# Optimization experiments

Hardware: AMD Instinct MI355X
Metric: run time of the kernel (lower is better)

The kernel has to match this reference:

```python
import jax, jax.numpy as jnp
import numpy as np

L, D, F, V = 24, 1024, 4096, 50277  # n_layer, n_embd, ffn hidden (4*D), vocab
RESCALE = 6


def _ln(x, w, b, eps=1e-5):
    m = jnp.mean(x, axis=-1, keepdims=True)
    v = jnp.mean(jnp.square(x - m), axis=-1, keepdims=True)
    return (x - m) * jax.lax.rsqrt(v + eps) * w + b


def setup_inputs() -> dict:
    key = jax.random.key(0)
    ks = iter(jax.random.split(key, 64))

    def nrm(shape, s=0.02):
        return jax.random.normal(next(ks), shape, jnp.float32) * s

    def uni(shape):
        return jax.random.uniform(next(ks), shape, jnp.float32)

    state = jnp.zeros((L, 5, D), jnp.float32).at[:, 4, :].set(-1e30)  # pp init
    return {
        "token_embd": jax.random.normal(next(ks), (D,), jnp.float32),
        "state": state,
        "emb_ln_w": jnp.ones((D,), jnp.float32),
        "emb_ln_b": jnp.zeros((D,), jnp.float32),
        "ln1_w": jnp.ones((L, D), jnp.float32),
        "ln1_b": jnp.zeros((L, D), jnp.float32),
        "ln2_w": jnp.ones((L, D), jnp.float32),
        "ln2_b": jnp.zeros((L, D), jnp.float32),
        "att_tmk": uni((L, D)),
        "att_tmv": uni((L, D)),
        "att_tmr": uni((L, D)),
        "att_tf": nrm((L, D), 0.5),
        "att_td": -jnp.exp(nrm((L, D), 0.5)),  # time_decay = -exp(w) at load
        "att_kw": nrm((L, D, D)),
        "att_vw": nrm((L, D, D)),
        "att_rw": nrm((L, D, D)),
        "att_ow": nrm((L, D, D)),
        "ffn_tmk": uni((L, D)),
        "ffn_tmr": uni((L, D)),
        "ffn_kw": nrm((L, F, D)),
        "ffn_vw": nrm((L, D, F)),
        "ffn_rw": nrm((L, D, D)),
        "out_ln_w": jnp.ones((D,), jnp.float32),
        "out_ln_b": jnp.zeros((D,), jnp.float32),
        "head_w": nrm((V, D)),
    }


def reference(token_embd, state, emb_ln_w, emb_ln_b, ln1_w, ln1_b, ln2_w, ln2_b,
              att_tmk, att_tmv, att_tmr, att_tf, att_td, att_kw, att_vw, att_rw,
              att_ow, ffn_tmk, ffn_tmr, ffn_kw, ffn_vw, ffn_rw,
              out_ln_w, out_ln_b, head_w):
    x0 = _ln(token_embd, emb_ln_w, emb_ln_b)  # encoder

    def layer(x, inputs):
        (i, st, l1w, l1b, l2w, l2b, tmk, tmv, tmr, tf, td,
         kw, vw, rw, ow, ftmk, ftmr, fkw, fvw, frw) = inputs
        # ---- time mixing ----
        xn = _ln(x, l1w, l1b)
        s_att, aa, bb, pp = st[1], st[2], st[3], st[4]
        xk = xn * tmk + s_att * (1 - tmk)
        xv = xn * tmv + s_att * (1 - tmv)
        xr = xn * tmr + s_att * (1 - tmr)
        r = jax.nn.sigmoid(rw @ xr)
        kk = kw @ xk
        vv = vw @ xv
        ww = tf + kk
        p = jnp.maximum(pp, ww)
        e1 = jnp.exp(pp - p)
        e2 = jnp.exp(ww - p)
        a = e1 * aa + e2 * vv
        b = e1 * bb + e2
        ww2 = pp + td
        p2 = jnp.maximum(ww2, kk)
        f1 = jnp.exp(ww2 - p2)
        f2 = jnp.exp(kk - p2)
        new_aa = f1 * aa + f2 * vv
        new_bb = f1 * bb + f2
        x = x + ow @ (r * (a / b))
        # ---- channel mixing ----
        xn2 = _ln(x, l2w, l2b)
        s_ffn = st[0]
        xk2 = xn2 * ftmk + s_ffn * (1 - ftmk)
        xr2 = xn2 * ftmr + s_ffn * (1 - ftmr)
        r2 = jax.nn.sigmoid(frw @ xr2)
        k2 = jnp.square(jax.nn.relu(fkw @ xk2))
        x = x + r2 * (fvw @ k2)
        # rescale every RESCALE layers
        x = jnp.where((i + 1) % RESCALE == 0, x * 0.5, x)
        new_st = jnp.stack([xn2, xn, new_aa, new_bb, p2])
        return x, new_st

    idx = jnp.arange(L)
    x, new_state = jax.lax.scan(
        layer, x0,
        (idx, state, ln1_w, ln1_b, ln2_w, ln2_b, att_tmk, att_tmv, att_tmr,
         att_tf, att_td, att_kw, att_vw, att_rw, att_ow, ffn_tmk, ffn_tmr,
         ffn_kw, ffn_vw, ffn_rw))
    logits = head_w @ _ln(x, out_ln_w, out_ln_b)  # decoder
    return logits, new_state
```

## Files before the change

kernel.cpp:

```cpp
#include <hip/hip_runtime.h>

#define DD 1024
#define FF 4096
#define LL 24
#define VV 50277
#define PFB 256

typedef float v4f __attribute__((ext_vector_type(4)));


__device__ __forceinline__ float wave_sum(float v) {
#pragma unroll
    for (int o = 32; o > 0; o >>= 1) v += __shfl_xor(v, o, 64);
    return v;
}

__device__ __forceinline__ float block_sum(float v, float* scr) {
    v = wave_sum(v);
    int w = threadIdx.x >> 6;
    __syncthreads();
    if ((threadIdx.x & 63) == 0) scr[w] = v;
    __syncthreads();
    return scr[0] + scr[1] + scr[2] + scr[3];
}

__device__ __forceinline__ v4f ln_vec(v4f xv, const float* __restrict__ w,
                                      const float* __restrict__ b, float* scr, int t) {
    float m = block_sum(xv[0] + xv[1] + xv[2] + xv[3], scr) * (1.0f / 1024.0f);
    v4f d = xv - m;
    float var = block_sum(d[0]*d[0] + d[1]*d[1] + d[2]*d[2] + d[3]*d[3], scr) * (1.0f / 1024.0f);
    float rs = rsqrtf(var + 1e-5f);
    v4f w4 = ((const v4f*)w)[t], b4 = ((const v4f*)b)[t];
    return d * rs * w4 + b4;
}

__device__ __forceinline__ v4f mixv(v4f n, v4f s, v4f m) { return n * m + s * (1.0f - m); }

__device__ __forceinline__ float dotv(v4f a, v4f x) {
    return fmaf(a[0], x[0], fmaf(a[1], x[1], fmaf(a[2], x[2], a[3] * x[3])));
}

struct Row { v4f a, b, c, d; };

__device__ __forceinline__ void row_load(Row& r, const float* p, int lane) {
    const v4f* q = (const v4f*)p;
    r.a = q[lane]; r.b = q[lane + 64]; r.c = q[lane + 128]; r.d = q[lane + 192];
}
__device__ __forceinline__ float row_dot(const Row& r, const v4f* v, int lane) {
    return dotv(r.a, v[lane]) + dotv(r.b, v[lane + 64]) +
           dotv(r.c, v[lane + 128]) + dotv(r.d, v[lane + 192]);
}


__device__ __forceinline__ void pf_region(const float* p, int nvec, int pb, int t) {
    if (p == nullptr || nvec <= 0) return;
    const v4f* q = (const v4f*)p;
    int chunk = (nvec + PFB - 1) / PFB;
    int lo = pb * chunk;
    int end = lo + chunk; if (end > nvec) end = nvec;
    int i = lo + t;
    v4f a0 = {0,0,0,0}, a1 = a0, a2 = a0, a3 = a0, a4 = a0, a5 = a0, a6 = a0, a7 = a0;
    for (; i + 1792 < end; i += 2048) {
        v4f t0 = q[i],        t1 = q[i + 256],  t2 = q[i + 512],  t3 = q[i + 768];
        v4f t4 = q[i + 1024], t5 = q[i + 1280], t6 = q[i + 1536], t7 = q[i + 1792];
        a0 += t0; a1 += t1; a2 += t2; a3 += t3;
        a4 += t4; a5 += t5; a6 += t6; a7 += t7;
    }
    for (; i < end; i += 256) a0 += q[i];
    a0 = (a0 + a1) + (a2 + a3) + ((a4 + a5) + (a6 + a7));
    asm volatile("" :: "v"(a0));
}


__global__ __launch_bounds__(256) void k1_timemix(
    const float* __restrict__ xin, const float* __restrict__ st,
    const float* __restrict__ enc_w, const float* __restrict__ enc_b,
    const float* __restrict__ l1w, const float* __restrict__ l1b,
    const float* __restrict__ tmk, const float* __restrict__ tmv,
    const float* __restrict__ tmr,
    const float* __restrict__ kw, const float* __restrict__ vw,
    const float* __restrict__ rw,
    float* __restrict__ kk, float* __restrict__ vv, float* __restrict__ rr,
    float* __restrict__ x0out, float* __restrict__ st_out,
    const float* pfa, int na, const float* pfb, int nb) {
    const int t = threadIdx.x;
    int b = blockIdx.x;
    if (b < PFB) { pf_region(pfa, na, b, t); pf_region(pfb, nb, b, t); return; }
    b -= PFB;
    __shared__ __align__(16) float s_k[DD], s_v[DD], s_r[DD];
    __shared__ float scr[4];
    const int lane = t & 63, w = t >> 6;

    v4f xv = ((const v4f*)xin)[t];
    if (enc_w) xv = ln_vec(xv, enc_w, enc_b, scr, t);
    if (x0out && b == 0) ((v4f*)x0out)[t] = xv;
    v4f n = ln_vec(xv, l1w, l1b, scr, t);
    if (b == 0) ((v4f*)(st_out + DD))[t] = n;
    {
        v4f sa = ((const v4f*)(st + DD))[t];
        ((v4f*)s_k)[t] = mixv(n, sa, ((const v4f*)tmk)[t]);
        ((v4f*)s_v)[t] = mixv(n, sa, ((const v4f*)tmv)[t]);
        ((v4f*)s_r)[t] = mixv(n, sa, ((const v4f*)tmr)[t]);
    }
    __syncthreads();

    const int ridx = b * 4 + w, m = ridx >> 10, row = ridx & 1023;
    Row W;
    row_load(W, (m == 0 ? kw : m == 1 ? vw : rw) + (size_t)row * DD, lane);
    const v4f* vec = (const v4f*)(m == 0 ? s_k : m == 1 ? s_v : s_r);
    float acc = wave_sum(row_dot(W, vec, lane));
    if (lane == 0) {
        if (m == 0)      kk[row] = acc;
        else if (m == 1) vv[row] = acc;
        else             rr[row] = 1.0f / (1.0f + expf(-acc));
    }
}


__global__ __launch_bounds__(256) void k2_wkv_out(
    const float* __restrict__ st, const float* __restrict__ tf,
    const float* __restrict__ td,
    const float* __restrict__ kk, const float* __restrict__ vv,
    const float* __restrict__ rr, const float* __restrict__ ow,
    float* __restrict__ x, float* __restrict__ st_out,
    const float* pfa, int na, const float* pfb, int nb) {
    const int t = threadIdx.x;
    int b = blockIdx.x;
    if (b < PFB) { pf_region(pfa, na, b, t); pf_region(pfb, nb, b, t); return; }
    b -= PFB;
    __shared__ __align__(16) float rab[DD];
    const int lane = t & 63, w = t >> 6;

    {
        v4f kx = ((const v4f*)kk)[t];
        v4f vx = ((const v4f*)vv)[t];
        v4f rx = ((const v4f*)rr)[t];
        v4f aa = ((const v4f*)(st + 2 * DD))[t];
        v4f bb = ((const v4f*)(st + 3 * DD))[t];
        v4f pp = ((const v4f*)(st + 4 * DD))[t];
        v4f tf4 = ((const v4f*)tf)[t];
        v4f td4 = ((const v4f*)td)[t];
        v4f rb, naa, nbb, np2;
#pragma unroll
        for (int c = 0; c < 4; ++c) {
            float kc = kx[c], vc = vx[c];
            float wwc = tf4[c] + kc;
            float p = fmaxf(pp[c], wwc);
            float e1 = expf(pp[c] - p), e2 = expf(wwc - p);
            rb[c] = rx[c] * ((e1 * aa[c] + e2 * vc) / (e1 * bb[c] + e2));
            float ww2 = pp[c] + td4[c];
            float p2 = fmaxf(ww2, kc);
            float f1 = expf(ww2 - p2), f2 = expf(kc - p2);
            naa[c] = f1 * aa[c] + f2 * vc;
            nbb[c] = f1 * bb[c] + f2;
            np2[c] = p2;
        }
        ((v4f*)rab)[t] = rb;
        if (b == 0) {
            ((v4f*)(st_out + 2 * DD))[t] = naa;
            ((v4f*)(st_out + 3 * DD))[t] = nbb;
            ((v4f*)(st_out + 4 * DD))[t] = np2;
        }
    }
    __syncthreads();

    const int row = b * 4 + w;
    Row W;
    row_load(W, ow + (size_t)row * DD, lane);
    float acc = wave_sum(row_dot(W, (const v4f*)rab, lane));
    if (lane == 0) x[row] += acc;
}


__global__ __launch_bounds__(256) void k3_ffn_kr(
    const float* __restrict__ x, const float* __restrict__ st,
    const float* __restrict__ l2w, const float* __restrict__ l2b,
    const float* __restrict__ ftmk, const float* __restrict__ ftmr,
    const float* __restrict__ fkw, const float* __restrict__ frw,
    float* __restrict__ k2, float* __restrict__ r2, float* __restrict__ st_out,
    const float* pfa, int na, const float* pfb, int nb) {
    const int t = threadIdx.x;
    int b = blockIdx.x;
    if (b < PFB) { pf_region(pfa, na, b, t); pf_region(pfb, nb, b, t); return; }
    b -= PFB;
    __shared__ __align__(16) float s_k[DD], s_r[DD];
    __shared__ float scr[4];
    const int lane = t & 63, w = t >> 6;

    v4f xv = ((const v4f*)x)[t];
    v4f n = ln_vec(xv, l2w, l2b, scr, t);
    if (b == 0) ((v4f*)st_out)[t] = n;
    {
        v4f sf = ((const v4f*)st)[t];
        ((v4f*)s_k)[t] = mixv(n, sf, ((const v4f*)ftmk)[t]);
        ((v4f*)s_r)[t] = mixv(n, sf, ((const v4f*)ftmr)[t]);
    }
    __syncthreads();

    const int ridx = b * 4 + w;
    const float* Wp;
    const v4f* vec;
    if (ridx < FF) { Wp = fkw + (size_t)ridx * DD; vec = (const v4f*)s_k; }
    else           { Wp = frw + (size_t)(ridx - FF) * DD; vec = (const v4f*)s_r; }
    Row W;
    row_load(W, Wp, lane);
    float acc = wave_sum(row_dot(W, vec, lane));
    if (lane == 0) {
        if (ridx < FF) { float rl = fmaxf(acc, 0.f); k2[ridx] = rl * rl; }
        else           r2[ridx - FF] = 1.0f / (1.0f + expf(-acc));
    }
}


__global__ __launch_bounds__(256) void k4_ffn_v(
    const float* __restrict__ fvw, const float* __restrict__ k2,
    const float* __restrict__ r2, float* __restrict__ x, float scale,
    const float* pfa, int na, const float* pfb, int nb) {
    const int t = threadIdx.x;
    int b = blockIdx.x;
    if (b < PFB) { pf_region(pfa, na, b, t); pf_region(pfb, nb, b, t); return; }
    b -= PFB;
    __shared__ __align__(16) float k2s[FF];
    const int lane = t & 63, w = t >> 6;
#pragma unroll
    for (int j = 0; j < 4; ++j)
        ((v4f*)k2s)[t + 256 * j] = ((const v4f*)k2)[t + 256 * j];
    __syncthreads();

    const int row = b * 4 + w;
    const v4f* W4 = (const v4f*)(fvw + (size_t)row * FF);
    const v4f* v4 = (const v4f*)k2s;
    float acc = 0.f;
#pragma unroll
    for (int j = 0; j < 16; ++j) {
        v4f a = W4[lane + 64 * j];
        v4f bx = v4[lane + 64 * j];
        acc = fmaf(a[0], bx[0], fmaf(a[1], bx[1], fmaf(a[2], bx[2], fmaf(a[3], bx[3], acc))));
    }
    acc = wave_sum(acc);
    if (lane == 0) x[row] = (x[row] + r2[row] * acc) * scale;
}


__global__ __launch_bounds__(256) void k_head(const float* __restrict__ head_w,
                                              const float* __restrict__ x,
                                              const float* __restrict__ olw,
                                              const float* __restrict__ olb,
                                              float* __restrict__ logits) {
    __shared__ __align__(16) float xs[DD];
    __shared__ float scr[4];
    const int t = threadIdx.x, lane = t & 63, w = t >> 6;
    const int row = blockIdx.x * 4 + w;
    Row W;
    if (row < VV) row_load(W, head_w + (size_t)row * DD, lane);
    v4f xv = ((const v4f*)x)[t];
    v4f nx = ln_vec(xv, olw, olb, scr, t);
    ((v4f*)xs)[t] = nx;
    __syncthreads();
    if (row < VV) {
        float acc = wave_sum(row_dot(W, (const v4f*)xs, lane));
        if (lane == 0) logits[row] = acc;
    }
}


extern "C" void kernel_launch(void* const* d_in, const int* in_sizes, int n_in,
                              void* d_out, int out_size, void* d_ws, size_t ws_size,
                              hipStream_t stream) {
    const float* token_embd = (const float*)d_in[0];
    const float* state      = (const float*)d_in[1];
    const float* emb_ln_w   = (const float*)d_in[2];
    const float* emb_ln_b   = (const float*)d_in[3];
    const float* ln1_w      = (const float*)d_in[4];
    const float* ln1_b      = (const float*)d_in[5];
    const float* ln2_w      = (const float*)d_in[6];
    const float* ln2_b      = (const float*)d_in[7];
    const float* att_tmk    = (const float*)d_in[8];
    const float* att_tmv    = (const float*)d_in[9];
    const float* att_tmr    = (const float*)d_in[10];
    const float* att_tf     = (const float*)d_in[11];
    const float* att_td     = (const float*)d_in[12];
    const float* att_kw     = (const float*)d_in[13];
    const float* att_vw     = (const float*)d_in[14];
    const float* att_rw     = (const float*)d_in[15];
    const float* att_ow     = (const float*)d_in[16];
    const float* ffn_tmk    = (const float*)d_in[17];
    const float* ffn_tmr    = (const float*)d_in[18];
    const float* ffn_kw     = (const float*)d_in[19];
    const float* ffn_vw     = (const float*)d_in[20];
    const float* ffn_rw     = (const float*)d_in[21];
    const float* out_ln_w   = (const float*)d_in[22];
    const float* out_ln_b   = (const float*)d_in[23];
    const float* head_w     = (const float*)d_in[24];

    float* logits = (float*)d_out;
    float* st_out_base = (float*)d_out + VV;

    float* ws  = (float*)d_ws;
    float* x   = ws;
    float* kk  = ws + 1024;
    float* vv  = ws + 2048;
    float* rr  = ws + 3072;
    float* k2b = ws + 4096;
    float* r2b = ws + 8192;

    const int V_D   = DD * DD / 4;
    const int V_FKH = FF * DD / 8;

    for (int i = 0; i < LL; ++i) {
        const float* st = state + (size_t)i * 5 * DD;
        float* sto = st_out_base + (size_t)i * 5 * DD;
        const float* kw_i  = att_kw + (size_t)i * DD * DD;
        const float* vw_i  = att_vw + (size_t)i * DD * DD;
        const float* rw_i  = att_rw + (size_t)i * DD * DD;
        const float* ow_i  = att_ow + (size_t)i * DD * DD;
        const float* fkw_i = ffn_kw + (size_t)i * FF * DD;
        const float* fvw_i = ffn_vw + (size_t)i * DD * FF;
        const float* frw_i = ffn_rw + (size_t)i * DD * DD;
        const bool last = (i == LL - 1);

        k1_timemix<<<PFB + 768, 256, 0, stream>>>(
            (i == 0) ? token_embd : x, st,
            (i == 0) ? emb_ln_w : nullptr, (i == 0) ? emb_ln_b : nullptr,
            ln1_w + i * DD, ln1_b + i * DD,
            att_tmk + i * DD, att_tmv + i * DD, att_tmr + i * DD,
            kw_i, vw_i, rw_i, kk, vv, rr,
            (i == 0) ? x : nullptr, sto,
            ow_i, V_D, fkw_i, V_FKH);

        k2_wkv_out<<<PFB + 256, 256, 0, stream>>>(
            st, att_tf + i * DD, att_td + i * DD, kk, vv, rr, ow_i, x, sto,
            fkw_i + (size_t)FF * DD / 2, V_FKH, frw_i, V_D);

        k3_ffn_kr<<<PFB + 1280, 256, 0, stream>>>(
            x, st, ln2_w + i * DD, ln2_b + i * DD,
            ffn_tmk + i * DD, ffn_tmr + i * DD, fkw_i, frw_i,
            k2b, r2b, sto,
            fvw_i, 2 * V_FKH,
            last ? nullptr : rw_i + DD * DD, last ? 0 : V_D);

        float scale = ((i + 1) % 6 == 0) ? 0.5f : 1.0f;
        k4_ffn_v<<<PFB + 256, 256, 0, stream>>>(
            fvw_i, k2b, r2b, x, scale,
            last ? nullptr : kw_i + DD * DD, last ? 0 : V_D,
            last ? nullptr : vw_i + DD * DD, last ? 0 : V_D);
    }

    k_head<<<(VV + 3) / 4, 256, 0, stream>>>(head_w, x, out_ln_w, out_ln_b, logits);
}
```

Baseline: 722.5 us.

## Fuse RWKV layer into two kernels with split-K atomics, drop prefetch blocks

Each layer's four kernels become two. kA computes the k/v/r projections, the WKV update and the output projection for a column slice, accumulating into per-layer buffers with atomics. kB fuses the FFN key/receptance matvecs with a column-sliced value matvec, also accumulated with atomics. The residual update is deferred into the next kernel's prologue, and the L2 prefetch blocks are removed. LayerNorm moves to a one-pass sum and sum-of-squares reduction. This cuts launches and intermediate round trips, at the cost of float atomics and a less numerically stable variance.

```diff
diff --git a/kernel.cpp b/kernel.cpp
--- a/kernel.cpp
+++ b/kernel.cpp
@@ -4,7 +4,6 @@
 #define FF 4096
 #define LL 24
 #define VV 50277
-#define PFB 256
 
 typedef float v4f __attribute__((ext_vector_type(4)));
 
@@ -15,23 +14,26 @@
     return v;
 }
 
-__device__ __forceinline__ float block_sum(float v, float* scr) {
-    v = wave_sum(v);
-    int w = threadIdx.x >> 6;
-    __syncthreads();
-    if ((threadIdx.x & 63) == 0) scr[w] = v;
-    __syncthreads();
-    return scr[0] + scr[1] + scr[2] + scr[3];
-}
-
-__device__ __forceinline__ v4f ln_vec(v4f xv, const float* __restrict__ w,
-                                      const float* __restrict__ b, float* scr, int t) {
-    float m = block_sum(xv[0] + xv[1] + xv[2] + xv[3], scr) * (1.0f / 1024.0f);
-    v4f d = xv - m;
-    float var = block_sum(d[0]*d[0] + d[1]*d[1] + d[2]*d[2] + d[3]*d[3], scr) * (1.0f / 1024.0f);
+template <int NW>
+__device__ __forceinline__ v4f ln_fast(v4f x, const float* __restrict__ w,
+                                       const float* __restrict__ b,
+                                       float* scr, int t, bool act) {
+    float s1 = act ? (x[0] + x[1] + x[2] + x[3]) : 0.f;
+    float s2 = act ? (x[0]*x[0] + x[1]*x[1] + x[2]*x[2] + x[3]*x[3]) : 0.f;
+    s1 = wave_sum(s1); s2 = wave_sum(s2);
+    int wv = t >> 6;
+    __syncthreads();
+    if ((t & 63) == 0) { scr[wv] = s1; scr[NW + wv] = s2; }
+    __syncthreads();
+    float S1 = 0.f, S2 = 0.f;
+#pragma unroll
+    for (int i = 0; i < NW; ++i) { S1 += scr[i]; S2 += scr[NW + i]; }
+    float m = S1 * (1.0f / 1024.0f);
+    float var = S2 * (1.0f / 1024.0f) - m * m;
     float rs = rsqrtf(var + 1e-5f);
-    v4f w4 = ((const v4f*)w)[t], b4 = ((const v4f*)b)[t];
-    return d * rs * w4 + b4;
+    v4f w4 = act ? ((const v4f*)w)[t] : (v4f){0.f, 0.f, 0.f, 0.f};
+    v4f b4 = act ? ((const v4f*)b)[t] : (v4f){0.f, 0.f, 0.f, 0.f};
+    return (x - m) * rs * w4 + b4;
 }
 
 __device__ __forceinline__ v4f mixv(v4f n, v4f s, v4f m) { return n * m + s * (1.0f - m); }
@@ -52,213 +54,167 @@
 }
 
 
-__device__ __forceinline__ void pf_region(const float* p, int nvec, int pb, int t) {
-    if (p == nullptr || nvec <= 0) return;
-    const v4f* q = (const v4f*)p;
-    int chunk = (nvec + PFB - 1) / PFB;
-    int lo = pb * chunk;
-    int end = lo + chunk; if (end > nvec) end = nvec;
-    int i = lo + t;
-    v4f a0 = {0,0,0,0}, a1 = a0, a2 = a0, a3 = a0, a4 = a0, a5 = a0, a6 = a0, a7 = a0;
-    for (; i + 1792 < end; i += 2048) {
-        v4f t0 = q[i],        t1 = q[i + 256],  t2 = q[i + 512],  t3 = q[i + 768];
-        v4f t4 = q[i + 1024], t5 = q[i + 1280], t6 = q[i + 1536], t7 = q[i + 1792];
-        a0 += t0; a1 += t1; a2 += t2; a3 += t3;
-        a4 += t4; a5 += t5; a6 += t6; a7 += t7;
-    }
-    for (; i < end; i += 256) a0 += q[i];
-    a0 = (a0 + a1) + (a2 + a3) + ((a4 + a5) + (a6 + a7));
-    asm volatile("" :: "v"(a0));
-}
-
-
-__global__ __launch_bounds__(256) void k1_timemix(
-    const float* __restrict__ xin, const float* __restrict__ st,
+__global__ __launch_bounds__(768, 3) void kA(
+    const float* __restrict__ xprev, const float* __restrict__ a1p,
+    const float* __restrict__ r2p, const float* __restrict__ sp, float scale_prev,
     const float* __restrict__ enc_w, const float* __restrict__ enc_b,
+    const float* __restrict__ st,
     const float* __restrict__ l1w, const float* __restrict__ l1b,
     const float* __restrict__ tmk, const float* __restrict__ tmv,
-    const float* __restrict__ tmr,
+    const float* __restrict__ tmr, const float* __restrict__ tf,
+    const float* __restrict__ td,
     const float* __restrict__ kw, const float* __restrict__ vw,
-    const float* __restrict__ rw,
-    float* __restrict__ kk, float* __restrict__ vv, float* __restrict__ rr,
-    float* __restrict__ x0out, float* __restrict__ st_out,
-    const float* pfa, int na, const float* pfb, int nb) {
-    const int t = threadIdx.x;
-    int b = blockIdx.x;
-    if (b < PFB) { pf_region(pfa, na, b, t); pf_region(pfb, nb, b, t); return; }
-    b -= PFB;
-    __shared__ __align__(16) float s_k[DD], s_v[DD], s_r[DD];
-    __shared__ float scr[4];
-    const int lane = t & 63, w = t >> 6;
-
-    v4f xv = ((const v4f*)xin)[t];
-    if (enc_w) xv = ln_vec(xv, enc_w, enc_b, scr, t);
-    if (x0out && b == 0) ((v4f*)x0out)[t] = xv;
-    v4f n = ln_vec(xv, l1w, l1b, scr, t);
-    if (b == 0) ((v4f*)(st_out + DD))[t] = n;
-    {
+    const float* __restrict__ rw, const float* __restrict__ ow,
+    float* __restrict__ A1i, float* __restrict__ xbuf_i, float* __restrict__ sto) {
+    __shared__ __align__(16) v4f s_mix[3][256];
+    __shared__ float kvrL[3][4];
+    __shared__ __align__(16) float rabL[4];
+    __shared__ float scr[24];
+    const int t = threadIdx.x, lane = t & 63, w = t >> 6, b = blockIdx.x;
+
+    const int m = w >> 2, ch4 = w & 3;
+    Row R;
+    row_load(R, (m == 0 ? kw : m == 1 ? vw : rw) + (size_t)(4 * b + ch4) * DD, lane);
+    v4f ow0 = *(const v4f*)(ow + (size_t)t * DD + 4 * b);
+    v4f ow1;
+    if (t < 256) ow1 = *(const v4f*)(ow + (size_t)(768 + t) * DD + 4 * b);
+
+    v4f xin = {0.f, 0.f, 0.f, 0.f};
+    if (t < 256) {
+        v4f xp = ((const v4f*)xprev)[t];
+        if (enc_w == nullptr) {
+            v4f a1 = ((const v4f*)a1p)[t];
+            v4f r2 = ((const v4f*)r2p)[t];
+            v4f s  = ((const v4f*)sp)[t];
+            xin = (xp + a1 + r2 * s) * scale_prev;
+        } else xin = xp;
+    }
+    if (enc_w) xin = ln_fast<12>(xin, enc_w, enc_b, scr, t, t < 256);
+
+    v4f xn = ln_fast<12>(xin, l1w, l1b, scr, t, t < 256);
+    if (t < 256) {
+        if (b == 0) {
+            ((v4f*)(sto + DD))[t] = xn;
+            ((v4f*)xbuf_i)[t] = xin;
+        }
         v4f sa = ((const v4f*)(st + DD))[t];
-        ((v4f*)s_k)[t] = mixv(n, sa, ((const v4f*)tmk)[t]);
-        ((v4f*)s_v)[t] = mixv(n, sa, ((const v4f*)tmv)[t]);
-        ((v4f*)s_r)[t] = mixv(n, sa, ((const v4f*)tmr)[t]);
-    }
-    __syncthreads();
-
-    const int ridx = b * 4 + w, m = ridx >> 10, row = ridx & 1023;
-    Row W;
-    row_load(W, (m == 0 ? kw : m == 1 ? vw : rw) + (size_t)row * DD, lane);
-    const v4f* vec = (const v4f*)(m == 0 ? s_k : m == 1 ? s_v : s_r);
-    float acc = wave_sum(row_dot(W, vec, lane));
-    if (lane == 0) {
-        if (m == 0)      kk[row] = acc;
-        else if (m == 1) vv[row] = acc;
-        else             rr[row] = 1.0f / (1.0f + expf(-acc));
-    }
-}
-
-
-__global__ __launch_bounds__(256) void k2_wkv_out(
-    const float* __restrict__ st, const float* __restrict__ tf,
-    const float* __restrict__ td,
-    const float* __restrict__ kk, const float* __restrict__ vv,
-    const float* __restrict__ rr, const float* __restrict__ ow,
-    float* __restrict__ x, float* __restrict__ st_out,
-    const float* pfa, int na, const float* pfb, int nb) {
-    const int t = threadIdx.x;
-    int b = blockIdx.x;
-    if (b < PFB) { pf_region(pfa, na, b, t); pf_region(pfb, nb, b, t); return; }
-    b -= PFB;
-    __shared__ __align__(16) float rab[DD];
-    const int lane = t & 63, w = t >> 6;
-
-    {
-        v4f kx = ((const v4f*)kk)[t];
-        v4f vx = ((const v4f*)vv)[t];
-        v4f rx = ((const v4f*)rr)[t];
-        v4f aa = ((const v4f*)(st + 2 * DD))[t];
-        v4f bb = ((const v4f*)(st + 3 * DD))[t];
-        v4f pp = ((const v4f*)(st + 4 * DD))[t];
-        v4f tf4 = ((const v4f*)tf)[t];
-        v4f td4 = ((const v4f*)td)[t];
-        v4f rb, naa, nbb, np2;
-#pragma unroll
-        for (int c = 0; c < 4; ++c) {
-            float kc = kx[c], vc = vx[c];
-            float wwc = tf4[c] + kc;
-            float p = fmaxf(pp[c], wwc);
-            float e1 = expf(pp[c] - p), e2 = expf(wwc - p);
-            rb[c] = rx[c] * ((e1 * aa[c] + e2 * vc) / (e1 * bb[c] + e2));
-            float ww2 = pp[c] + td4[c];
-            float p2 = fmaxf(ww2, kc);
-            float f1 = expf(ww2 - p2), f2 = expf(kc - p2);
-            naa[c] = f1 * aa[c] + f2 * vc;
-            nbb[c] = f1 * bb[c] + f2;
-            np2[c] = p2;
-        }
-        ((v4f*)rab)[t] = rb;
-        if (b == 0) {
-            ((v4f*)(st_out + 2 * DD))[t] = naa;
-            ((v4f*)(st_out + 3 * DD))[t] = nbb;
-            ((v4f*)(st_out + 4 * DD))[t] = np2;
-        }
-    }
-    __syncthreads();
-
-    const int row = b * 4 + w;
-    Row W;
-    row_load(W, ow + (size_t)row * DD, lane);
-    float acc = wave_sum(row_dot(W, (const v4f*)rab, lane));
-    if (lane == 0) x[row] += acc;
-}
-
-
-__global__ __launch_bounds__(256) void k3_ffn_kr(
-    const float* __restrict__ x, const float* __restrict__ st,
+        s_mix[0][t] = mixv(xn, sa, ((const v4f*)tmk)[t]);
+        s_mix[1][t] = mixv(xn, sa, ((const v4f*)tmv)[t]);
+        s_mix[2][t] = mixv(xn, sa, ((const v4f*)tmr)[t]);
+    }
+    __syncthreads();
+
+    {
+        float acc = wave_sum(row_dot(R, &s_mix[m][0], lane));
+        if (lane == 0) kvrL[m][ch4] = acc;
+    }
+    __syncthreads();
+
+    if (t < 4) {
+        const int c = 4 * b + t;
+        float kk = kvrL[0][t], vv = kvrL[1][t];
+        float rr = 1.0f / (1.0f + expf(-kvrL[2][t]));
+        float aa = st[2 * DD + c], bb = st[3 * DD + c], pp = st[4 * DD + c];
+        float tfv = tf[c], tdv = td[c];
+        float ww = tfv + kk;
+        float p = fmaxf(pp, ww);
+        float e1 = expf(pp - p), e2 = expf(ww - p);
+        rabL[t] = rr * ((e1 * aa + e2 * vv) / (e1 * bb + e2));
+        float ww2 = pp + tdv;
+        float p2 = fmaxf(ww2, kk);
+        float f1 = expf(ww2 - p2), f2 = expf(kk - p2);
+        sto[2 * DD + c] = f1 * aa + f2 * vv;
+        sto[3 * DD + c] = f1 * bb + f2;
+        sto[4 * DD + c] = p2;
+    }
+    __syncthreads();
+
+    {
+        v4f rab4 = *(const v4f*)rabL;
+        atomicAdd(&A1i[t], dotv(ow0, rab4));
+        if (t < 256) atomicAdd(&A1i[768 + t], dotv(ow1, rab4));
+    }
+}
+
+
+__global__ __launch_bounds__(256, 2) void kB(
+    const float* __restrict__ xbuf_i, const float* __restrict__ A1i,
+    const float* __restrict__ st,
     const float* __restrict__ l2w, const float* __restrict__ l2b,
     const float* __restrict__ ftmk, const float* __restrict__ ftmr,
-    const float* __restrict__ fkw, const float* __restrict__ frw,
-    float* __restrict__ k2, float* __restrict__ r2, float* __restrict__ st_out,
-    const float* pfa, int na, const float* pfb, int nb) {
-    const int t = threadIdx.x;
-    int b = blockIdx.x;
-    if (b < PFB) { pf_region(pfa, na, b, t); pf_region(pfb, nb, b, t); return; }
-    b -= PFB;
-    __shared__ __align__(16) float s_k[DD], s_r[DD];
-    __shared__ float scr[4];
-    const int lane = t & 63, w = t >> 6;
-
-    v4f xv = ((const v4f*)x)[t];
-    v4f n = ln_vec(xv, l2w, l2b, scr, t);
-    if (b == 0) ((v4f*)st_out)[t] = n;
+    const float* __restrict__ fkw, const float* __restrict__ fvw,
+    const float* __restrict__ frw,
+    float* __restrict__ Si, float* __restrict__ r2o, float* __restrict__ sto) {
+    __shared__ __align__(16) v4f s_k[256], s_r[256];
+    __shared__ __align__(16) float k2L[16];
+    __shared__ float scr[8];
+    const int t = threadIdx.x, lane = t & 63, w = t >> 6, b = blockIdx.x;
+
+    const float* fkbase = fkw + (size_t)(16 * b + 4 * w) * DD;
+    Row R0;
+    row_load(R0, fkbase, lane);
+
+    v4f xv = ((const v4f*)xbuf_i)[t] + ((const v4f*)A1i)[t];
+    v4f xn2 = ln_fast<4>(xv, l2w, l2b, scr, t, true);
+    if (b == 0) ((v4f*)sto)[t] = xn2;
     {
         v4f sf = ((const v4f*)st)[t];
-        ((v4f*)s_k)[t] = mixv(n, sf, ((const v4f*)ftmk)[t]);
-        ((v4f*)s_r)[t] = mixv(n, sf, ((const v4f*)ftmr)[t]);
-    }
-    __syncthreads();
-
-    const int ridx = b * 4 + w;
-    const float* Wp;
-    const v4f* vec;
-    if (ridx < FF) { Wp = fkw + (size_t)ridx * DD; vec = (const v4f*)s_k; }
-    else           { Wp = frw + (size_t)(ridx - FF) * DD; vec = (const v4f*)s_r; }
-    Row W;
-    row_load(W, Wp, lane);
-    float acc = wave_sum(row_dot(W, vec, lane));
-    if (lane == 0) {
-        if (ridx < FF) { float rl = fmaxf(acc, 0.f); k2[ridx] = rl * rl; }
-        else           r2[ridx - FF] = 1.0f / (1.0f + expf(-acc));
-    }
-}
-
-
-__global__ __launch_bounds__(256) void k4_ffn_v(
-    const float* __restrict__ fvw, const float* __restrict__ k2,
-    const float* __restrict__ r2, float* __restrict__ x, float scale,
-    const float* pfa, int na, const float* pfb, int nb) {
-    const int t = threadIdx.x;
-    int b = blockIdx.x;
-    if (b < PFB) { pf_region(pfa, na, b, t); pf_region(pfb, nb, b, t); return; }
-    b -= PFB;
-    __shared__ __align__(16) float k2s[FF];
-    const int lane = t & 63, w = t >> 6;
-#pragma unroll
-    for (int j = 0; j < 4; ++j)
-        ((v4f*)k2s)[t + 256 * j] = ((const v4f*)k2)[t + 256 * j];
-    __syncthreads();
-
-    const int row = b * 4 + w;
-    const v4f* W4 = (const v4f*)(fvw + (size_t)row * FF);
-    const v4f* v4 = (const v4f*)k2s;
-    float acc = 0.f;
-#pragma unroll
-    for (int j = 0; j < 16; ++j) {
-        v4f a = W4[lane + 64 * j];
-        v4f bx = v4[lane + 64 * j];
-        acc = fmaf(a[0], bx[0], fmaf(a[1], bx[1], fmaf(a[2], bx[2], fmaf(a[3], bx[3], acc))));
-    }
-    acc = wave_sum(acc);
-    if (lane == 0) x[row] = (x[row] + r2[row] * acc) * scale;
-}
-
-
-__global__ __launch_bounds__(256) void k_head(const float* __restrict__ head_w,
-                                              const float* __restrict__ x,
-                                              const float* __restrict__ olw,
-                                              const float* __restrict__ olb,
-                                              float* __restrict__ logits) {
-    __shared__ __align__(16) float xs[DD];
-    __shared__ float scr[4];
+        s_k[t] = mixv(xn2, sf, ((const v4f*)ftmk)[t]);
+        s_r[t] = mixv(xn2, sf, ((const v4f*)ftmr)[t]);
+    }
+    __syncthreads();
+
+    {
+        float a0 = wave_sum(row_dot(R0, &s_k[0], lane));
+        if (lane == 0) { float rl = fmaxf(a0, 0.f); k2L[4 * w] = rl * rl; }
+#pragma unroll
+        for (int r = 1; r < 4; ++r) {
+            Row R;
+            row_load(R, fkbase + (size_t)r * DD, lane);
+            float a = wave_sum(row_dot(R, &s_k[0], lane));
+            if (lane == 0) { float rl = fmaxf(a, 0.f); k2L[4 * w + r] = rl * rl; }
+        }
+        Row Rf;
+        row_load(Rf, frw + (size_t)(4 * b + w) * DD, lane);
+        float ar = wave_sum(row_dot(Rf, &s_r[0], lane));
+        if (lane == 0) r2o[4 * b + w] = 1.0f / (1.0f + expf(-ar));
+    }
+    __syncthreads();
+
+    {
+        v4f k0 = ((const v4f*)k2L)[0], k1 = ((const v4f*)k2L)[1];
+        v4f k2v = ((const v4f*)k2L)[2], k3 = ((const v4f*)k2L)[3];
+#pragma unroll
+        for (int jj = 0; jj < 4; ++jj) {
+            int j = t + 256 * jj;
+            const v4f* q = (const v4f*)(fvw + (size_t)j * FF + 16 * b);
+            float part = dotv(q[0], k0) + dotv(q[1], k1) + dotv(q[2], k2v) + dotv(q[3], k3);
+            atomicAdd(&Si[j], part);
+        }
+    }
+}
+
+
+__global__ __launch_bounds__(256) void k_head(
+    const float* __restrict__ head_w,
+    const float* __restrict__ x23, const float* __restrict__ a1p,
+    const float* __restrict__ r2p, const float* __restrict__ sp, float scale,
+    const float* __restrict__ olw, const float* __restrict__ olb,
+    float* __restrict__ logits) {
+    __shared__ __align__(16) v4f xs[256];
+    __shared__ float scr[8];
     const int t = threadIdx.x, lane = t & 63, w = t >> 6;
     const int row = blockIdx.x * 4 + w;
     Row W;
     if (row < VV) row_load(W, head_w + (size_t)row * DD, lane);
-    v4f xv = ((const v4f*)x)[t];
-    v4f nx = ln_vec(xv, olw, olb, scr, t);
-    ((v4f*)xs)[t] = nx;
+
+    v4f xf = (((const v4f*)x23)[t] + ((const v4f*)a1p)[t] +
+              ((const v4f*)r2p)[t] * ((const v4f*)sp)[t]) * scale;
+    v4f nx = ln_fast<4>(xf, olw, olb, scr, t, true);
+    xs[t] = nx;
     __syncthreads();
     if (row < VV) {
-        float acc = wave_sum(row_dot(W, (const v4f*)xs, lane));
+        float acc = wave_sum(row_dot(W, &xs[0], lane));
         if (lane == 0) logits[row] = acc;
     }
 }
@@ -296,55 +252,40 @@
     float* logits = (float*)d_out;
     float* st_out_base = (float*)d_out + VV;
 
-    float* ws  = (float*)d_ws;
-    float* x   = ws;
-    float* kk  = ws + 1024;
-    float* vv  = ws + 2048;
-    float* rr  = ws + 3072;
-    float* k2b = ws + 4096;
-    float* r2b = ws + 8192;
-
-    const int V_D   = DD * DD / 4;
-    const int V_FKH = FF * DD / 8;
+    float* ws   = (float*)d_ws;
+    float* A1   = ws;
+    float* S    = ws + 24 * DD;
+    float* r2b  = ws + 48 * DD;
+    float* xbuf = ws + 72 * DD;
+
+    hipMemsetAsync(A1, 0, 48 * DD * sizeof(float), stream);
 
     for (int i = 0; i < LL; ++i) {
         const float* st = state + (size_t)i * 5 * DD;
         float* sto = st_out_base + (size_t)i * 5 * DD;
-        const float* kw_i  = att_kw + (size_t)i * DD * DD;
-        const float* vw_i  = att_vw + (size_t)i * DD * DD;
-        const float* rw_i  = att_rw + (size_t)i * DD * DD;
-        const float* ow_i  = att_ow + (size_t)i * DD * DD;
-        const float* fkw_i = ffn_kw + (size_t)i * FF * DD;
-        const float* fvw_i = ffn_vw + (size_t)i * DD * FF;
-        const float* frw_i = ffn_rw + (size_t)i * DD * DD;
-        const bool last = (i == LL - 1);
-
-        k1_timemix<<<PFB + 768, 256, 0, stream>>>(
-            (i == 0) ? token_embd : x, st,
+        const float scale_prev = (i > 0 && i % 6 == 0) ? 0.5f : 1.0f;
+
+        kA<<<256, 768, 0, stream>>>(
+            (i == 0) ? token_embd : xbuf + (i - 1) * DD,
+            A1 + (i - 1) * DD, r2b + (i - 1) * DD, S + (i - 1) * DD, scale_prev,
             (i == 0) ? emb_ln_w : nullptr, (i == 0) ? emb_ln_b : nullptr,
-            ln1_w + i * DD, ln1_b + i * DD,
+            st, ln1_w + i * DD, ln1_b + i * DD,
             att_tmk + i * DD, att_tmv + i * DD, att_tmr + i * DD,
-            kw_i, vw_i, rw_i, kk, vv, rr,
-            (i == 0) ? x : nullptr, sto,
-            ow_i, V_D, fkw_i, V_FKH);
-
-        k2_wkv_out<<<PFB + 256, 256, 0, stream>>>(
-            st, att_tf + i * DD, att_td + i * DD, kk, vv, rr, ow_i, x, sto,
-            fkw_i + (size_t)FF * DD / 2, V_FKH, frw_i, V_D);
-
-        k3_ffn_kr<<<PFB + 1280, 256, 0, stream>>>(
-            x, st, ln2_w + i * DD, ln2_b + i * DD,
-            ffn_tmk + i * DD, ffn_tmr + i * DD, fkw_i, frw_i,
-            k2b, r2b, sto,
-            fvw_i, 2 * V_FKH,
-            last ? nullptr : rw_i + DD * DD, last ? 0 : V_D);
-
-        float scale = ((i + 1) % 6 == 0) ? 0.5f : 1.0f;
-        k4_ffn_v<<<PFB + 256, 256, 0, stream>>>(
-            fvw_i, k2b, r2b, x, scale,
-            last ? nullptr : kw_i + DD * DD, last ? 0 : V_D,
-            last ? nullptr : vw_i + DD * DD, last ? 0 : V_D);
-    }
-
-    k_head<<<(VV + 3) / 4, 256, 0, stream>>>(head_w, x, out_ln_w, out_ln_b, logits);
-}
+            att_tf + i * DD, att_td + i * DD,
+            att_kw + (size_t)i * DD * DD, att_vw + (size_t)i * DD * DD,
+            att_rw + (size_t)i * DD * DD, att_ow + (size_t)i * DD * DD,
+            A1 + i * DD, xbuf + i * DD, sto);
+
+        kB<<<256, 256, 0, stream>>>(
+            xbuf + i * DD, A1 + i * DD, st,
+            ln2_w + i * DD, ln2_b + i * DD,
+            ffn_tmk + i * DD, ffn_tmr + i * DD,
+            ffn_kw + (size_t)i * FF * DD, ffn_vw + (size_t)i * DD * FF,
+            ffn_rw + (size_t)i * DD * DD,
+            S + i * DD, r2b + i * DD, sto);
+    }
+
+    k_head<<<(VV + 3) / 4, 256, 0, stream>>>(
+        head_w, xbuf + 23 * DD, A1 + 23 * DD, r2b + 23 * DD, S + 23 * DD, 0.5f,
+        out_ln_w, out_ln_b, logits);
+}
```

After: 896.1 us. 1.24x slower.

## Replace cross-kernel L2 prefetch blocks with in-kernel early weight loads

Applied to the files above, without the earlier changes.

Removes the extra prefetch blocks that each kernel used to pull the next stage's weights into cache. Instead, every kernel now issues its own weight-row loads first, pinned in registers with an asm barrier, so that DRAM latency overlaps the LayerNorm and mixing prologue. LayerNorm is also changed to a single-pass sum and sum-of-squares reduction with one fewer block sync. This gives up overlap between consecutive kernels and uses the less numerically stable E[x^2]-m^2 variance form.

```diff
diff --git a/kernel.cpp b/kernel.cpp
--- a/kernel.cpp
+++ b/kernel.cpp
@@ -4,7 +4,6 @@
 #define FF 4096
 #define LL 24
 #define VV 50277
-#define PFB 256
 
 typedef float v4f __attribute__((ext_vector_type(4)));
 
@@ -15,23 +14,23 @@
     return v;
 }
 
-__device__ __forceinline__ float block_sum(float v, float* scr) {
-    v = wave_sum(v);
-    int w = threadIdx.x >> 6;
-    __syncthreads();
-    if ((threadIdx.x & 63) == 0) scr[w] = v;
-    __syncthreads();
-    return scr[0] + scr[1] + scr[2] + scr[3];
-}
-
-__device__ __forceinline__ v4f ln_vec(v4f xv, const float* __restrict__ w,
-                                      const float* __restrict__ b, float* scr, int t) {
-    float m = block_sum(xv[0] + xv[1] + xv[2] + xv[3], scr) * (1.0f / 1024.0f);
-    v4f d = xv - m;
-    float var = block_sum(d[0]*d[0] + d[1]*d[1] + d[2]*d[2] + d[3]*d[3], scr) * (1.0f / 1024.0f);
+__device__ __forceinline__ v4f ln_fast(v4f x, const float* __restrict__ w,
+                                       const float* __restrict__ b,
+                                       float* scr, int t) {
+    float s1 = x[0] + x[1] + x[2] + x[3];
+    float s2 = x[0]*x[0] + x[1]*x[1] + x[2]*x[2] + x[3]*x[3];
+    s1 = wave_sum(s1); s2 = wave_sum(s2);
+    int wv = t >> 6;
+    __syncthreads();
+    if ((t & 63) == 0) { scr[wv] = s1; scr[4 + wv] = s2; }
+    __syncthreads();
+    float S1 = scr[0] + scr[1] + scr[2] + scr[3];
+    float S2 = scr[4] + scr[5] + scr[6] + scr[7];
+    float m = S1 * (1.0f / 1024.0f);
+    float var = S2 * (1.0f / 1024.0f) - m * m;
     float rs = rsqrtf(var + 1e-5f);
     v4f w4 = ((const v4f*)w)[t], b4 = ((const v4f*)b)[t];
-    return d * rs * w4 + b4;
+    return (x - m) * rs * w4 + b4;
 }
 
 __device__ __forceinline__ v4f mixv(v4f n, v4f s, v4f m) { return n * m + s * (1.0f - m); }
@@ -46,29 +45,12 @@
     const v4f* q = (const v4f*)p;
     r.a = q[lane]; r.b = q[lane + 64]; r.c = q[lane + 128]; r.d = q[lane + 192];
 }
+__device__ __forceinline__ void row_pin(Row& r) {
+    asm volatile("" : "+v"(r.a), "+v"(r.b), "+v"(r.c), "+v"(r.d));
+}
 __device__ __forceinline__ float row_dot(const Row& r, const v4f* v, int lane) {
     return dotv(r.a, v[lane]) + dotv(r.b, v[lane + 64]) +
            dotv(r.c, v[lane + 128]) + dotv(r.d, v[lane + 192]);
-}
-
-
-__device__ __forceinline__ void pf_region(const float* p, int nvec, int pb, int t) {
-    if (p == nullptr || nvec <= 0) return;
-    const v4f* q = (const v4f*)p;
-    int chunk = (nvec + PFB - 1) / PFB;
-    int lo = pb * chunk;
-    int end = lo + chunk; if (end > nvec) end = nvec;
-    int i = lo + t;
-    v4f a0 = {0,0,0,0}, a1 = a0, a2 = a0, a3 = a0, a4 = a0, a5 = a0, a6 = a0, a7 = a0;
-    for (; i + 1792 < end; i += 2048) {
-        v4f t0 = q[i],        t1 = q[i + 256],  t2 = q[i + 512],  t3 = q[i + 768];
-        v4f t4 = q[i + 1024], t5 = q[i + 1280], t6 = q[i + 1536], t7 = q[i + 1792];
-        a0 += t0; a1 += t1; a2 += t2; a3 += t3;
-        a4 += t4; a5 += t5; a6 += t6; a7 += t7;
-    }
-    for (; i < end; i += 256) a0 += q[i];
-    a0 = (a0 + a1) + (a2 + a3) + ((a4 + a5) + (a6 + a7));
-    asm volatile("" :: "v"(a0));
 }
 
 
@@ -81,33 +63,30 @@
     const float* __restrict__ kw, const float* __restrict__ vw,
     const float* __restrict__ rw,
     float* __restrict__ kk, float* __restrict__ vv, float* __restrict__ rr,
-    float* __restrict__ x0out, float* __restrict__ st_out,
-    const float* pfa, int na, const float* pfb, int nb) {
-    const int t = threadIdx.x;
-    int b = blockIdx.x;
-    if (b < PFB) { pf_region(pfa, na, b, t); pf_region(pfb, nb, b, t); return; }
-    b -= PFB;
-    __shared__ __align__(16) float s_k[DD], s_v[DD], s_r[DD];
-    __shared__ float scr[4];
-    const int lane = t & 63, w = t >> 6;
+    float* __restrict__ x0out, float* __restrict__ st_out) {
+    __shared__ __align__(16) v4f s_k[256], s_v[256], s_r[256];
+    __shared__ float scr[8];
+    const int t = threadIdx.x, lane = t & 63, w = t >> 6, b = blockIdx.x;
+
+    const int ridx = 4 * b + w, m = ridx >> 10, row = ridx & 1023;
+    Row W;
+    row_load(W, (m == 0 ? kw : m == 1 ? vw : rw) + (size_t)row * DD, lane);
+    row_pin(W);
 
     v4f xv = ((const v4f*)xin)[t];
-    if (enc_w) xv = ln_vec(xv, enc_w, enc_b, scr, t);
+    if (enc_w) xv = ln_fast(xv, enc_w, enc_b, scr, t);
     if (x0out && b == 0) ((v4f*)x0out)[t] = xv;
-    v4f n = ln_vec(xv, l1w, l1b, scr, t);
+    v4f n = ln_fast(xv, l1w, l1b, scr, t);
     if (b == 0) ((v4f*)(st_out + DD))[t] = n;
     {
         v4f sa = ((const v4f*)(st + DD))[t];
-        ((v4f*)s_k)[t] = mixv(n, sa, ((const v4f*)tmk)[t]);
-        ((v4f*)s_v)[t] = mixv(n, sa, ((const v4f*)tmv)[t]);
-        ((v4f*)s_r)[t] = mixv(n, sa, ((const v4f*)tmr)[t]);
-    }
-    __syncthreads();
-
-    const int ridx = b * 4 + w, m = ridx >> 10, row = ridx & 1023;
-    Row W;
-    row_load(W, (m == 0 ? kw : m == 1 ? vw : rw) + (size_t)row * DD, lane);
-    const v4f* vec = (const v4f*)(m == 0 ? s_k : m == 1 ? s_v : s_r);
+        s_k[t] = mixv(n, sa, ((const v4f*)tmk)[t]);
+        s_v[t] = mixv(n, sa, ((const v4f*)tmv)[t]);
+        s_r[t] = mixv(n, sa, ((const v4f*)tmr)[t]);
+    }
+    __syncthreads();
+
+    const v4f* vec = (m == 0) ? s_k : (m == 1) ? s_v : s_r;
     float acc = wave_sum(row_dot(W, vec, lane));
     if (lane == 0) {
         if (m == 0)      kk[row] = acc;
@@ -122,14 +101,14 @@
     const float* __restrict__ td,
     const float* __restrict__ kk, const float* __restrict__ vv,
     const float* __restrict__ rr, const float* __restrict__ ow,
-    float* __restrict__ x, float* __restrict__ st_out,
-    const float* pfa, int na, const float* pfb, int nb) {
-    const int t = threadIdx.x;
-    int b = blockIdx.x;
-    if (b < PFB) { pf_region(pfa, na, b, t); pf_region(pfb, nb, b, t); return; }
-    b -= PFB;
-    __shared__ __align__(16) float rab[DD];
-    const int lane = t & 63, w = t >> 6;
+    float* __restrict__ x, float* __restrict__ st_out) {
+    __shared__ __align__(16) v4f rab[256];
+    const int t = threadIdx.x, lane = t & 63, w = t >> 6, b = blockIdx.x;
+
+    const int row = 4 * b + w;
+    Row W;
+    row_load(W, ow + (size_t)row * DD, lane);
+    row_pin(W);
 
     {
         v4f kx = ((const v4f*)kk)[t];
@@ -155,7 +134,7 @@
             nbb[c] = f1 * bb[c] + f2;
             np2[c] = p2;
         }
-        ((v4f*)rab)[t] = rb;
+        rab[t] = rb;
         if (b == 0) {
             ((v4f*)(st_out + 2 * DD))[t] = naa;
             ((v4f*)(st_out + 3 * DD))[t] = nbb;
@@ -164,10 +143,7 @@
     }
     __syncthreads();
 
-    const int row = b * 4 + w;
-    Row W;
-    row_load(W, ow + (size_t)row * DD, lane);
-    float acc = wave_sum(row_dot(W, (const v4f*)rab, lane));
+    float acc = wave_sum(row_dot(W, &rab[0], lane));
     if (lane == 0) x[row] += acc;
 }
 
@@ -177,33 +153,28 @@
     const float* __restrict__ l2w, const float* __restrict__ l2b,
     const float* __restrict__ ftmk, const float* __restrict__ ftmr,
     const float* __restrict__ fkw, const float* __restrict__ frw,
-    float* __restrict__ k2, float* __restrict__ r2, float* __restrict__ st_out,
-    const float* pfa, int na, const float* pfb, int nb) {
-    const int t = threadIdx.x;
-    int b = blockIdx.x;
-    if (b < PFB) { pf_region(pfa, na, b, t); pf_region(pfb, nb, b, t); return; }
-    b -= PFB;
-    __shared__ __align__(16) float s_k[DD], s_r[DD];
-    __shared__ float scr[4];
-    const int lane = t & 63, w = t >> 6;
+    float* __restrict__ k2, float* __restrict__ r2, float* __restrict__ st_out) {
+    __shared__ __align__(16) v4f s_k[256], s_r[256];
+    __shared__ float scr[8];
+    const int t = threadIdx.x, lane = t & 63, w = t >> 6, b = blockIdx.x;
+
+    const int ridx = 4 * b + w;
+    Row W;
+    row_load(W, (ridx < FF ? fkw + (size_t)ridx * DD
+                           : frw + (size_t)(ridx - FF) * DD), lane);
+    row_pin(W);
 
     v4f xv = ((const v4f*)x)[t];
-    v4f n = ln_vec(xv, l2w, l2b, scr, t);
+    v4f n = ln_fast(xv, l2w, l2b, scr, t);
     if (b == 0) ((v4f*)st_out)[t] = n;
     {
         v4f sf = ((const v4f*)st)[t];
-        ((v4f*)s_k)[t] = mixv(n, sf, ((const v4f*)ftmk)[t]);
-        ((v4f*)s_r)[t] = mixv(n, sf, ((const v4f*)ftmr)[t]);
-    }
-    __syncthreads();
-
-    const int ridx = b * 4 + w;
-    const float* Wp;
-    const v4f* vec;
-    if (ridx < FF) { Wp = fkw + (size_t)ridx * DD; vec = (const v4f*)s_k; }
-    else           { Wp = frw + (size_t)(ridx - FF) * DD; vec = (const v4f*)s_r; }
-    Row W;
-    row_load(W, Wp, lane);
+        s_k[t] = mixv(n, sf, ((const v4f*)ftmk)[t]);
+        s_r[t] = mixv(n, sf, ((const v4f*)ftmr)[t]);
+    }
+    __syncthreads();
+
+    const v4f* vec = (ridx < FF) ? s_k : s_r;
     float acc = wave_sum(row_dot(W, vec, lane));
     if (lane == 0) {
         if (ridx < FF) { float rl = fmaxf(acc, 0.f); k2[ridx] = rl * rl; }
@@ -214,28 +185,30 @@
 
 __global__ __launch_bounds__(256) void k4_ffn_v(
     const float* __restrict__ fvw, const float* __restrict__ k2,
-    const float* __restrict__ r2, float* __restrict__ x, float scale,
-    const float* pfa, int na, const float* pfb, int nb) {
-    const int t = threadIdx.x;
-    int b = blockIdx.x;
-    if (b < PFB) { pf_region(pfa, na, b, t); pf_region(pfb, nb, b, t); return; }
-    b -= PFB;
-    __shared__ __align__(16) float k2s[FF];
-    const int lane = t & 63, w = t >> 6;
+    const float* __restrict__ r2, float* __restrict__ x, float scale) {
+    __shared__ __align__(16) v4f k2s[1024];
+    const int t = threadIdx.x, lane = t & 63, w = t >> 6, b = blockIdx.x;
+    const int row = 4 * b + w;
+    const v4f* W4 = (const v4f*)(fvw + (size_t)row * FF);
+
+    v4f h0 = W4[lane],       h1 = W4[lane + 64],  h2 = W4[lane + 128], h3 = W4[lane + 192];
+    v4f h4 = W4[lane + 256], h5 = W4[lane + 320], h6 = W4[lane + 384], h7 = W4[lane + 448];
+    asm volatile("" : "+v"(h0), "+v"(h1), "+v"(h2), "+v"(h3),
+                      "+v"(h4), "+v"(h5), "+v"(h6), "+v"(h7));
+
 #pragma unroll
     for (int j = 0; j < 4; ++j)
-        ((v4f*)k2s)[t + 256 * j] = ((const v4f*)k2)[t + 256 * j];
-    __syncthreads();
-
-    const int row = b * 4 + w;
-    const v4f* W4 = (const v4f*)(fvw + (size_t)row * FF);
-    const v4f* v4 = (const v4f*)k2s;
-    float acc = 0.f;
+        k2s[t + 256 * j] = ((const v4f*)k2)[t + 256 * j];
+    __syncthreads();
+
+    float acc = dotv(h0, k2s[lane])       + dotv(h1, k2s[lane + 64]) +
+                dotv(h2, k2s[lane + 128]) + dotv(h3, k2s[lane + 192]) +
+                dotv(h4, k2s[lane + 256]) + dotv(h5, k2s[lane + 320]) +
+                dotv(h6, k2s[lane + 384]) + dotv(h7, k2s[lane + 448]);
 #pragma unroll
-    for (int j = 0; j < 16; ++j) {
+    for (int j = 8; j < 16; ++j) {
         v4f a = W4[lane + 64 * j];
-        v4f bx = v4[lane + 64 * j];
-        acc = fmaf(a[0], bx[0], fmaf(a[1], bx[1], fmaf(a[2], bx[2], fmaf(a[3], bx[3], acc))));
+        acc += dotv(a, k2s[lane + 64 * j]);
     }
     acc = wave_sum(acc);
     if (lane == 0) x[row] = (x[row] + r2[row] * acc) * scale;
@@ -247,18 +220,19 @@
                                               const float* __restrict__ olw,
                                               const float* __restrict__ olb,
                                               float* __restrict__ logits) {
-    __shared__ __align__(16) float xs[DD];
-    __shared__ float scr[4];
+    __shared__ __align__(16) v4f xs[256];
+    __shared__ float scr[8];
     const int t = threadIdx.x, lane = t & 63, w = t >> 6;
     const int row = blockIdx.x * 4 + w;
     Row W;
-    if (row < VV) row_load(W, head_w + (size_t)row * DD, lane);
+    if (row < VV) { row_load(W, head_w + (size_t)row * DD, lane); row_pin(W); }
+
     v4f xv = ((const v4f*)x)[t];
-    v4f nx = ln_vec(xv, olw, olb, scr, t);
-    ((v4f*)xs)[t] = nx;
+    v4f nx = ln_fast(xv, olw, olb, scr, t);
+    xs[t] = nx;
     __syncthreads();
     if (row < VV) {
-        float acc = wave_sum(row_dot(W, (const v4f*)xs, lane));
+        float acc = wave_sum(row_dot(W, &xs[0], lane));
         if (lane == 0) logits[row] = acc;
     }
 }
@@ -304,46 +278,32 @@
     float* k2b = ws + 4096;
     float* r2b = ws + 8192;
 
-    const int V_D   = DD * DD / 4;
-    const int V_FKH = FF * DD / 8;
-
     for (int i = 0; i < LL; ++i) {
         const float* st = state + (size_t)i * 5 * DD;
         float* sto = st_out_base + (size_t)i * 5 * DD;
-        const float* kw_i  = att_kw + (size_t)i * DD * DD;
-        const float* vw_i  = att_vw + (size_t)i * DD * DD;
-        const float* rw_i  = att_rw + (size_t)i * DD * DD;
-        const float* ow_i  = att_ow + (size_t)i * DD * DD;
-        const float* fkw_i = ffn_kw + (size_t)i * FF * DD;
-        const float* fvw_i = ffn_vw + (size_t)i * DD * FF;
-        const float* frw_i = ffn_rw + (size_t)i * DD * DD;
-        const bool last = (i == LL - 1);
-
-        k1_timemix<<<PFB + 768, 256, 0, stream>>>(
+
+        k1_timemix<<<768, 256, 0, stream>>>(
             (i == 0) ? token_embd : x, st,
             (i == 0) ? emb_ln_w : nullptr, (i == 0) ? emb_ln_b : nullptr,
             ln1_w + i * DD, ln1_b + i * DD,
             att_tmk + i * DD, att_tmv + i * DD, att_tmr + i * DD,
-            kw_i, vw_i, rw_i, kk, vv, rr,
-            (i == 0) ? x : nullptr, sto,
-            ow_i, V_D, fkw_i, V_FKH);
-
-        k2_wkv_out<<<PFB + 256, 256, 0, stream>>>(
-            st, att_tf + i * DD, att_td + i * DD, kk, vv, rr, ow_i, x, sto,
-            fkw_i + (size_t)FF * DD / 2, V_FKH, frw_i, V_D);
-
-        k3_ffn_kr<<<PFB + 1280, 256, 0, stream>>>(
+            att_kw + (size_t)i * DD * DD, att_vw + (size_t)i * DD * DD,
+            att_rw + (size_t)i * DD * DD,
+            kk, vv, rr, (i == 0) ? x : nullptr, sto);
+
+        k2_wkv_out<<<256, 256, 0, stream>>>(
+            st, att_tf + i * DD, att_td + i * DD, kk, vv, rr,
+            att_ow + (size_t)i * DD * DD, x, sto);
+
+        k3_ffn_kr<<<1280, 256, 0, stream>>>(
             x, st, ln2_w + i * DD, ln2_b + i * DD,
-            ffn_tmk + i * DD, ffn_tmr + i * DD, fkw_i, frw_i,
-            k2b, r2b, sto,
-            fvw_i, 2 * V_FKH,
-            last ? nullptr : rw_i + DD * DD, last ? 0 : V_D);
+            ffn_tmk + i * DD, ffn_tmr + i * DD,
+            ffn_kw + (size_t)i * FF * DD, ffn_rw + (size_t)i * DD * DD,
+            k2b, r2b, sto);
 
         float scale = ((i + 1) % 6 == 0) ? 0.5f : 1.0f;
-        k4_ffn_v<<<PFB + 256, 256, 0, stream>>>(
-            fvw_i, k2b, r2b, x, scale,
-            last ? nullptr : kw_i + DD * DD, last ? 0 : V_D,
-            last ? nullptr : vw_i + DD * DD, last ? 0 : V_D);
+        k4_ffn_v<<<256, 256, 0, stream>>>(
+            ffn_vw + (size_t)i * DD * FF, k2b, r2b, x, scale);
     }
 
     k_head<<<(VV + 3) / 4, 256, 0, stream>>>(head_w, x, out_ln_w, out_ln_b, logits);
```

New measurement: 595.8 us. -17.5%, faster.
